# Performance work log

Measured on AMD Instinct MI355X. Metric: run time of the kernel, lower is better.

The kernel has to match this reference:

```python
import jax, jax.numpy as jnp
import numpy as np

B, L, C = 8, 1_000_000, 4


def _spiral_size(length: int) -> int:
    # size = round(sqrt(L / (pi/4 * 0.7)) / 2) * 2 + 1  (odd, size^2 >= L)
    s = np.sqrt(length / (np.pi / 4.0 * 0.7))
    return int(np.round(s / 2.0)) * 2 + 1


def _spiral_perm(size: int, length: int):
    """Grid slot index for each signal position (first `length` of argsort(phi2))."""
    PI = jnp.float32(np.pi)
    rnge = jnp.arange(size, dtype=jnp.float32) - size / 2.0 + 0.5
    x1, x2 = jnp.meshgrid(rnge, rnge)  # 'xy' indexing, same as tf.meshgrid default
    r = jnp.sqrt(x1 * x1 + x2 * x2)
    phi = jnp.arccos(x1 / r)                      # NaN at center (0/0)
    phi = jnp.where(jnp.isnan(phi), 0.0, phi)
    phi = phi * jnp.sign(x2)
    phi = phi + jnp.where((x2 == 0.0) & (x1 < 0.0), PI, 0.0)
    phi2 = jnp.round(r) * 2.0 * PI + phi          # spiral ordering key
    return jnp.argsort(phi2.reshape(-1))[:length]


def setup_inputs() -> dict:
    key = jax.random.key(0)
    return {"inputs": jax.random.normal(key, (B, L, C), dtype=jnp.float32)}


def reference(inputs):
    b, l, c = inputs.shape
    size = _spiral_size(l)
    perm = _spiral_perm(size, l)  # [l] unique grid slots
    # One-pass scatter of the signal into the dense size*size spiral grid
    grid = jnp.zeros((b, size * size, c), dtype=inputs.dtype).at[:, perm, :].set(inputs)
    return grid.reshape(b, size, size, c)
```

## Files before the change

kernel.cpp:

```cpp
#include <hip/hip_runtime.h>
#include <cstdint>
#include <utility>

#define SIZE 1349
#define HALF 674
#define N2 (SIZE*SIZE)
#define LSIG 1000000
#define NB 8
#define NRINGS 601
#define CAP 5376
#define MBUCKET 2048

constexpr long long isqrt_c(long long n) {
    if (n <= 0) return 0;
    long long x = 1;
    while (x * x <= n) x <<= 1;
    long long r = 0;
    for (long long b = x; b > 0; b >>= 1) { long long c = r + b; if (c * c <= n) r = c; }
    return r;
}
constexpr uint32_t rowcnt_c(int k, int y) {
    if (k == 0) return (y == 0) ? 1u : 0u;
    long long yy = (long long)y * y;
    long long Bv = (long long)k * (k + 1) - yy;
    if (Bv < 0) return 0u;
    long long h = isqrt_c(Bv); if (h > HALF) h = HALF;
    long long Av = (long long)k * (k - 1) + 1 - yy;
    if (Av <= 0) return (uint32_t)(2 * h + 1);
    long long f = isqrt_c(Av);
    long long lo = (f * f == Av) ? f : f + 1;
    if (lo > h) return 0u;
    return (uint32_t)(2 * (h - lo + 1));
}
constexpr uint32_t ringcnt_c(int k) {
    int ym = (k < HALF) ? k : HALF;
    uint32_t s = 0;
    for (int y = -ym; y <= ym; ++y) s += rowcnt_c(k, y);
    return s;
}
template<int K> struct RC { static constexpr uint32_t v = ringcnt_c(K); };
template<int K> struct OF { static constexpr uint32_t v = OF<K - 1>::v + RC<K - 1>::v; };
template<>      struct OF<0> { static constexpr uint32_t v = 0u; };

struct OffArr { uint32_t a[NRINGS]; };
template<int... I>
constexpr OffArr mkoff(std::integer_sequence<int, I...>) { return {{ OF<I>::v... }}; }

constexpr OffArr HOFF = mkoff(std::make_integer_sequence<int, NRINGS>{});

constexpr int klive_c() {
    for (int k = 0; k < NRINGS; ++k) if (HOFF.a[k] >= LSIG) return k;
    return NRINGS;
}
constexpr int KLIVE = klive_c();
constexpr uint32_t NTHRESH = (uint32_t)((long long)KLIVE * (KLIVE - 1) + 1);
constexpr uint32_t maxcnt_c() {
    uint32_t m = 0;
    for (int k = 0; k < KLIVE; ++k) { uint32_t c = HOFF.a[k + 1] - HOFF.a[k]; if (c > m) m = c; }
    return m;
}
static_assert(KLIVE < NRINGS - 1, "ring table too small");
static_assert(KLIVE <= HALF, "ymax clamp assumption broken");
static_assert(maxcnt_c() <= CAP, "CAP too small");
static_assert(HOFF.a[KLIVE] < LSIG + CAP, "T2 sizing");

__device__ __constant__ OffArr RING_OFF = mkoff(std::make_integer_sequence<int, NRINGS>{});

__device__ __forceinline__ int isqrt_i(int n) {
    int s = (int)sqrtf((float)n);
    while (s > 0 && s * s > n) s--;
    while ((s + 1) * (s + 1) <= n) s++;
    return s;
}

__device__ __forceinline__ int row_interval(int k, int y, int* xlo, int* xhi) {
    if (k == 0) { if (y == 0) { *xhi = 0; return 1; } return 0; }
    int yy = y * y;
    int B = k * (k + 1) - yy;
    if (B < 0) return 0;
    int h = isqrt_i(B);
    if (h > HALF) h = HALF;
    int A = k * (k - 1) + 1 - yy;
    *xhi = h;
    if (A <= 0) return 1;
    int f = isqrt_i(A);
    int lo = (f * f == A) ? f : f + 1;
    if (lo > h) return 0;
    *xlo = lo;
    return 2;
}

__device__ __forceinline__ int bucket_of(uint32_t kb, float tt) {
    const float PI_F = 3.14159265358979323846f;
    const float SC = 325.94932f;
    float p2 = __uint_as_float(kb);
    float u = (p2 - tt) + PI_F;
    int b = (int)(u * SC);
    return min(max(b, 0), MBUCKET - 1);
}

__device__ __forceinline__ uint32_t lds_append(uint32_t* nT) {
    unsigned long long m = __ballot(1);
    int lane = threadIdx.x & 63;
    int leader = __ffsll(m) - 1;
    uint32_t base = 0;
    if (lane == leader) base = atomicAdd(nT, (uint32_t)__popcll(m));
    base = __shfl(base, leader);
    return base + (uint32_t)__popcll(m & ((1ull << lane) - 1ull));
}

__device__ __forceinline__ void emit(int k, int x, int y, float tt,
                                     uint64_t* T, uint32_t* cnt, uint32_t* nT) {
#pragma clang fp contract(off)
    const float PI_F = 3.14159265358979323846f;
    uint32_t kp, kn = 0;
    if (y == 0) {
        float phi = (x < 0) ? PI_F : 0.0f;
        kp = __float_as_uint(tt + phi);
    } else {
        int nn = x * x + y * y;
        float rr = sqrtf((float)nn);
        float q = (float)x / rr;
        float ac = (float)::acos((double)q);
        kp = __float_as_uint(tt + ac);
        kn = __float_as_uint(tt - ac);
    }
    uint32_t gx = (uint32_t)(x + HALF);
    uint32_t gp = (uint32_t)(y + HALF) * SIZE + gx;
    uint32_t p = lds_append(nT);
    T[p] = ((uint64_t)kp << 32) | gp;
    atomicAdd(&cnt[bucket_of(kp, tt)], 1u);
    if (y > 0) {
        uint32_t gn = (uint32_t)(HALF - y) * SIZE + gx;
        uint32_t p2 = lds_append(nT);
        T[p2] = ((uint64_t)kn << 32) | gn;
        atomicAdd(&cnt[bucket_of(kn, tt)], 1u);
    }
}

__global__ __launch_bounds__(1024) void k_rank(uint32_t* __restrict__ rank,
                                               uint64_t* __restrict__ T2) {
#pragma clang fp contract(off)
    __shared__ uint64_t T[CAP];
    __shared__ uint32_t cnt[MBUCKET];
    __shared__ uint32_t boff[MBUCKET];
    __shared__ uint32_t ps[1024];
    __shared__ uint32_t nT;
    const float PI_F = 3.14159265358979323846f;
    int k = (KLIVE - 1) - (int)blockIdx.x;
    int t = threadIdx.x;
    if (k == 0) { if (t == 0) rank[HALF * SIZE + HALF] = 0u; return; }
    uint32_t off = RING_OFF.a[k];
    int n = (int)(RING_OFF.a[k + 1] - off);
    float tt = (2.0f * (float)k) * PI_F;

    cnt[2 * t] = 0u; cnt[2 * t + 1] = 0u;
    if (t == 0) nT = 0u;
    __syncthreads();

    int capy = (k >= 32) ? (k - 8) : (k + 1);
    int Bk = k * (k + 1), Ak = k * (k - 1) + 1;
    int nmain = 2 * capy;
    int w = 0, ncap = 0;
    if (capy <= k) { w = isqrt_i(Bk - capy * capy); ncap = 2 * w + 1; }
    int ntot = nmain + ncap;
    for (int task = t; task < ntot; task += 1024) {
        if (task < nmain) {
            int y = task >> 1, side = task & 1;
            int xlo = 0, xhi = 0;
            int kind = row_interval(k, y, &xlo, &xhi);
            if (kind == 0) continue;
            int xs, xe;
            if (side == 0) { xs = -xhi; xe = (kind == 1) ? -1 : -xlo; if (xe < xs) continue; }
            else          { xs = (kind == 1) ? 0 : xlo; xe = xhi; }
            for (int x = xs; x <= xe; ++x) emit(k, x, y, tt, T, cnt, &nT);
        } else {
            int x = (task - nmain) - w;
            int xx = x * x;
            int yhi = isqrt_i(Bk - xx);
            int aa = Ak - xx;
            int ylo = capy;
            if (aa > 0) {
                int f = isqrt_i(aa);
                int lo = (f * f == aa) ? f : f + 1;
                if (lo > ylo) ylo = lo;
            }
            for (int y = ylo; y <= yhi; ++y) emit(k, x, y, tt, T, cnt, &nT);
        }
    }
    __syncthreads();

    uint32_t c0 = cnt[2 * t], c1 = cnt[2 * t + 1];
    uint32_t s = c0 + c1;
    ps[t] = s;
    __syncthreads();
    for (int d = 1; d < 1024; d <<= 1) {
        uint32_t x = (t >= d) ? ps[t - d] : 0u;
        __syncthreads();
        ps[t] += x;
        __syncthreads();
    }
    uint32_t excl = ps[t] - s;
    boff[2 * t] = excl;
    boff[2 * t + 1] = excl + c0;
    __syncthreads();

    uint64_t* __restrict__ T2r = T2 + off;
    for (int i = t; i < n; i += 1024) {
        uint64_t v = T[i];
        int b = bucket_of((uint32_t)(v >> 32), tt);
        uint32_t p = atomicAdd(&boff[b], 1u);
        T2r[p] = v;
    }
    __syncthreads();

    for (int i = t; i < n; i += 1024) {
        uint64_t v = T[i];
        int b = bucket_of((uint32_t)(v >> 32), tt);
        uint32_t end = boff[b];
        uint32_t start = end - cnt[b];
        uint32_t c = 0;
        for (uint32_t j = start; j < end; ++j) c += (T2r[j] < v) ? 1u : 0u;
        rank[(uint32_t)v] = off + start + c;
    }
}

typedef float vfloat4 __attribute__((ext_vector_type(4)));

#define TW 16
#define TH 16

__global__ __launch_bounds__(256) void k_gather(const vfloat4* __restrict__ in,
                                                const uint32_t* __restrict__ rank,
                                                vfloat4* __restrict__ out) {
    int tx = threadIdx.x & (TW - 1);
    int ty = threadIdx.x / TW;
    int col = blockIdx.x * TW + tx;
    int row = blockIdx.y * TH + ty;
    int b = blockIdx.z;
    if (col >= SIZE || row >= SIZE) return;
    int g = row * SIZE + col;
    int dx = col - HALF, dy = row - HALF;
    uint32_t nn = (uint32_t)(dx * dx + dy * dy);
    uint32_t q = 0xFFFFFFFFu;
    if (nn < NTHRESH) q = rank[g];
    if (q < LSIG) {
        vfloat4 v = in[b * LSIG + (int)q];
        __builtin_nontemporal_store(v, &out[b * N2 + g]);
    } else {
        vfloat4 z = {0.f, 0.f, 0.f, 0.f};
        __builtin_nontemporal_store(z, &out[b * N2 + g]);
    }
}

extern "C" void kernel_launch(void* const* d_in, const int* in_sizes, int n_in,
                              void* d_out, int out_size, void* d_ws, size_t ws_size,
                              hipStream_t stream) {
    const float* in = (const float*)d_in[0];
    float* out = (float*)d_out;
    uint8_t* ws = (uint8_t*)d_ws;

    uint32_t* rank = (uint32_t*)ws;
    uint64_t* T2   = (uint64_t*)(ws + 16 * 1024 * 1024);

    k_rank<<<KLIVE, 1024, 0, stream>>>(rank, T2);

    dim3 gb((SIZE + TW - 1) / TW, (SIZE + TH - 1) / TH, NB);
    k_gather<<<gb, 256, 0, stream>>>((const vfloat4*)in, rank, (vfloat4*)out);
}
```

Baseline: 407.1 us.

## Enumerate ring twice to bucket-sort in LDS; batch gather rows per thread

The rank kernel drops the global T2 scratch buffer. It enumerates each ring twice, once to count bucket sizes and once to scatter entries directly into bucketed LDS positions, so the rank comparison reads shared memory instead of global memory. The old cap/row load-balancing split is also replaced by simple per-row tasks, which may leave long rows unbalanced, and the acos is now computed twice. The gather kernel now uses 32x32 tiles with 4 rows per thread so several rank loads and input loads are in flight at once.

```diff
diff --git a/kernel.cpp b/kernel.cpp
--- a/kernel.cpp
+++ b/kernel.cpp
@@ -62,7 +62,6 @@
 static_assert(KLIVE < NRINGS - 1, "ring table too small");
 static_assert(KLIVE <= HALF, "ymax clamp assumption broken");
 static_assert(maxcnt_c() <= CAP, "CAP too small");
-static_assert(HOFF.a[KLIVE] < LSIG + CAP, "T2 sizing");
 
 __device__ __constant__ OffArr RING_OFF = mkoff(std::make_integer_sequence<int, NRINGS>{});
 
@@ -99,95 +98,71 @@
     return min(max(b, 0), MBUCKET - 1);
 }
 
-__device__ __forceinline__ uint32_t lds_append(uint32_t* nT) {
-    unsigned long long m = __ballot(1);
-    int lane = threadIdx.x & 63;
-    int leader = __ffsll(m) - 1;
-    uint32_t base = 0;
-    if (lane == leader) base = atomicAdd(nT, (uint32_t)__popcll(m));
-    base = __shfl(base, leader);
-    return base + (uint32_t)__popcll(m & ((1ull << lane) - 1ull));
-}
-
-__device__ __forceinline__ void emit(int k, int x, int y, float tt,
-                                     uint64_t* T, uint32_t* cnt, uint32_t* nT) {
+template<int PHASE>
+__device__ __forceinline__ void enum_ring(int k, int ymaxv, float tt, int t,
+                                          uint32_t* cnt, uint32_t* boff, uint64_t* T) {
 #pragma clang fp contract(off)
     const float PI_F = 3.14159265358979323846f;
-    uint32_t kp, kn = 0;
-    if (y == 0) {
-        float phi = (x < 0) ? PI_F : 0.0f;
-        kp = __float_as_uint(tt + phi);
-    } else {
-        int nn = x * x + y * y;
-        float rr = sqrtf((float)nn);
-        float q = (float)x / rr;
-        float ac = (float)::acos((double)q);
-        kp = __float_as_uint(tt + ac);
-        kn = __float_as_uint(tt - ac);
-    }
-    uint32_t gx = (uint32_t)(x + HALF);
-    uint32_t gp = (uint32_t)(y + HALF) * SIZE + gx;
-    uint32_t p = lds_append(nT);
-    T[p] = ((uint64_t)kp << 32) | gp;
-    atomicAdd(&cnt[bucket_of(kp, tt)], 1u);
-    if (y > 0) {
-        uint32_t gn = (uint32_t)(HALF - y) * SIZE + gx;
-        uint32_t p2 = lds_append(nT);
-        T[p2] = ((uint64_t)kn << 32) | gn;
-        atomicAdd(&cnt[bucket_of(kn, tt)], 1u);
-    }
-}
-
-__global__ __launch_bounds__(1024) void k_rank(uint32_t* __restrict__ rank,
-                                               uint64_t* __restrict__ T2) {
+    int ntask = 2 * (ymaxv + 1);
+    for (int task = t; task < ntask; task += 1024) {
+        int y = task >> 1, side = task & 1;
+        int xlo = 0, xhi = 0;
+        int kind = row_interval(k, y, &xlo, &xhi);
+        if (kind == 0) continue;
+        int xs, xe;
+        if (side == 0) {
+            xs = -xhi; xe = (kind == 1) ? -1 : -xlo;
+            if (xe < xs) continue;
+        } else {
+            xs = (kind == 1) ? 0 : xlo; xe = xhi;
+        }
+        for (int x = xs; x <= xe; ++x) {
+            uint32_t kp, kn = 0;
+            if (y == 0) {
+                float phi = (x < 0) ? PI_F : 0.0f;
+                kp = __float_as_uint(tt + phi);
+            } else {
+                int nn = x * x + y * y;
+                float rr = sqrtf((float)nn);
+                float q = (float)x / rr;
+                float ac = (float)::acos((double)q);
+                kp = __float_as_uint(tt + ac);
+                kn = __float_as_uint(tt - ac);
+            }
+            uint32_t gx = (uint32_t)(x + HALF);
+            uint32_t gp = (uint32_t)(y + HALF) * SIZE + gx;
+            int bp = bucket_of(kp, tt);
+            if (PHASE == 0) atomicAdd(&cnt[bp], 1u);
+            else { uint32_t p = atomicAdd(&boff[bp], 1u); T[p] = ((uint64_t)kp << 32) | gp; }
+            if (y > 0) {
+                uint32_t gn = (uint32_t)(HALF - y) * SIZE + gx;
+                int bn = bucket_of(kn, tt);
+                if (PHASE == 0) atomicAdd(&cnt[bn], 1u);
+                else { uint32_t p = atomicAdd(&boff[bn], 1u); T[p] = ((uint64_t)kn << 32) | gn; }
+            }
+        }
+    }
+}
+
+__global__ __launch_bounds__(1024) void k_rank(uint32_t* __restrict__ rank) {
 #pragma clang fp contract(off)
     __shared__ uint64_t T[CAP];
     __shared__ uint32_t cnt[MBUCKET];
     __shared__ uint32_t boff[MBUCKET];
     __shared__ uint32_t ps[1024];
-    __shared__ uint32_t nT;
     const float PI_F = 3.14159265358979323846f;
     int k = (KLIVE - 1) - (int)blockIdx.x;
     int t = threadIdx.x;
     if (k == 0) { if (t == 0) rank[HALF * SIZE + HALF] = 0u; return; }
     uint32_t off = RING_OFF.a[k];
     int n = (int)(RING_OFF.a[k + 1] - off);
+    int ymaxv = min(k, HALF);
     float tt = (2.0f * (float)k) * PI_F;
 
     cnt[2 * t] = 0u; cnt[2 * t + 1] = 0u;
-    if (t == 0) nT = 0u;
-    __syncthreads();
-
-    int capy = (k >= 32) ? (k - 8) : (k + 1);
-    int Bk = k * (k + 1), Ak = k * (k - 1) + 1;
-    int nmain = 2 * capy;
-    int w = 0, ncap = 0;
-    if (capy <= k) { w = isqrt_i(Bk - capy * capy); ncap = 2 * w + 1; }
-    int ntot = nmain + ncap;
-    for (int task = t; task < ntot; task += 1024) {
-        if (task < nmain) {
-            int y = task >> 1, side = task & 1;
-            int xlo = 0, xhi = 0;
-            int kind = row_interval(k, y, &xlo, &xhi);
-            if (kind == 0) continue;
-            int xs, xe;
-            if (side == 0) { xs = -xhi; xe = (kind == 1) ? -1 : -xlo; if (xe < xs) continue; }
-            else          { xs = (kind == 1) ? 0 : xlo; xe = xhi; }
-            for (int x = xs; x <= xe; ++x) emit(k, x, y, tt, T, cnt, &nT);
-        } else {
-            int x = (task - nmain) - w;
-            int xx = x * x;
-            int yhi = isqrt_i(Bk - xx);
-            int aa = Ak - xx;
-            int ylo = capy;
-            if (aa > 0) {
-                int f = isqrt_i(aa);
-                int lo = (f * f == aa) ? f : f + 1;
-                if (lo > ylo) ylo = lo;
-            }
-            for (int y = ylo; y <= yhi; ++y) emit(k, x, y, tt, T, cnt, &nT);
-        }
-    }
+    __syncthreads();
+
+    enum_ring<0>(k, ymaxv, tt, t, cnt, boff, T);
     __syncthreads();
 
     uint32_t c0 = cnt[2 * t], c1 = cnt[2 * t + 1];
@@ -205,52 +180,57 @@
     boff[2 * t + 1] = excl + c0;
     __syncthreads();
 
-    uint64_t* __restrict__ T2r = T2 + off;
+    enum_ring<1>(k, ymaxv, tt, t, cnt, boff, T);
+    __syncthreads();
+
     for (int i = t; i < n; i += 1024) {
         uint64_t v = T[i];
-        int b = bucket_of((uint32_t)(v >> 32), tt);
-        uint32_t p = atomicAdd(&boff[b], 1u);
-        T2r[p] = v;
-    }
-    __syncthreads();
-
-    for (int i = t; i < n; i += 1024) {
-        uint64_t v = T[i];
-        int b = bucket_of((uint32_t)(v >> 32), tt);
+        uint32_t kb = (uint32_t)(v >> 32);
+        int b = bucket_of(kb, tt);
         uint32_t end = boff[b];
         uint32_t start = end - cnt[b];
         uint32_t c = 0;
-        for (uint32_t j = start; j < end; ++j) c += (T2r[j] < v) ? 1u : 0u;
+        for (uint32_t j = start; j < end; ++j) c += (T[j] < v) ? 1u : 0u;
         rank[(uint32_t)v] = off + start + c;
     }
 }
 
 typedef float vfloat4 __attribute__((ext_vector_type(4)));
-
-#define TW 16
-#define TH 16
 
 __global__ __launch_bounds__(256) void k_gather(const vfloat4* __restrict__ in,
                                                 const uint32_t* __restrict__ rank,
                                                 vfloat4* __restrict__ out) {
-    int tx = threadIdx.x & (TW - 1);
-    int ty = threadIdx.x / TW;
-    int col = blockIdx.x * TW + tx;
-    int row = blockIdx.y * TH + ty;
+    int tx = threadIdx.x & 31;
+    int ty = threadIdx.x >> 5;
+    int col = blockIdx.x * 32 + tx;
+    if (col >= SIZE) return;
+    int row0 = blockIdx.y * 32 + ty;
     int b = blockIdx.z;
-    if (col >= SIZE || row >= SIZE) return;
-    int g = row * SIZE + col;
-    int dx = col - HALF, dy = row - HALF;
-    uint32_t nn = (uint32_t)(dx * dx + dy * dy);
-    uint32_t q = 0xFFFFFFFFu;
-    if (nn < NTHRESH) q = rank[g];
-    if (q < LSIG) {
-        vfloat4 v = in[b * LSIG + (int)q];
-        __builtin_nontemporal_store(v, &out[b * N2 + g]);
-    } else {
+    const vfloat4* __restrict__ inb = in + (size_t)b * LSIG;
+    vfloat4* __restrict__ outb = out + (size_t)b * N2;
+    int dx = col - HALF;
+
+    uint32_t q[4]; int g[4]; bool ok[4];
+#pragma unroll
+    for (int j = 0; j < 4; ++j) {
+        int row = row0 + 8 * j;
+        ok[j] = (row < SIZE);
+        g[j] = row * SIZE + col;
+        int dy = row - HALF;
+        uint32_t nn = (uint32_t)(dx * dx + dy * dy);
+        q[j] = 0xFFFFFFFFu;
+        if (ok[j] && nn < NTHRESH) q[j] = rank[g[j]];
+    }
+    vfloat4 v[4];
+#pragma unroll
+    for (int j = 0; j < 4; ++j) {
         vfloat4 z = {0.f, 0.f, 0.f, 0.f};
-        __builtin_nontemporal_store(z, &out[b * N2 + g]);
-    }
+        v[j] = z;
+        if (q[j] < LSIG) v[j] = inb[(int)q[j]];
+    }
+#pragma unroll
+    for (int j = 0; j < 4; ++j)
+        if (ok[j]) __builtin_nontemporal_store(v[j], &outb[g[j]]);
 }
 
 extern "C" void kernel_launch(void* const* d_in, const int* in_sizes, int n_in,
@@ -261,10 +241,9 @@
     uint8_t* ws = (uint8_t*)d_ws;
 
     uint32_t* rank = (uint32_t*)ws;
-    uint64_t* T2   = (uint64_t*)(ws + 16 * 1024 * 1024);
-
-    k_rank<<<KLIVE, 1024, 0, stream>>>(rank, T2);
-
-    dim3 gb((SIZE + TW - 1) / TW, (SIZE + TH - 1) / TH, NB);
+
+    k_rank<<<KLIVE, 1024, 0, stream>>>(rank);
+
+    dim3 gb((SIZE + 31) / 32, (SIZE + 31) / 32, NB);
     k_gather<<<gb, 256, 0, stream>>>((const vfloat4*)in, rank, (vfloat4*)out);
 }
```

New measurement: 377.1 us. 7.4% less time.
